# Optimization experiments

Measured on AMD Instinct MI355X. Metric: run time of the kernel, lower is better.

## Reference

```python
import jax, jax.numpy as jnp
import numpy as np

B, N, DIM = 2, 2048, 1024
H, DH = 16, 64
INNER = H * DH
SCALE = DH ** -0.5


def rotate_half(x):
    x1, x2 = jnp.split(x, 2, axis=-1)
    return jnp.concatenate((-x2, x1), axis=-1)


def apply_rotary(pos, t):
    # pos: [n, dh] broadcast against t: [b, h, n, dh]
    return t * jnp.cos(pos) + rotate_half(t) * jnp.sin(pos)


def setup_inputs() -> dict:
    key = jax.random.key(0)
    ks = jax.random.split(key, 5)
    x = jax.random.normal(ks[0], (B, N, DIM), dtype=jnp.float32)
    rotary_emb = jax.random.normal(ks[1], (N, DH), dtype=jnp.float32)
    w_qkv = jax.random.normal(ks[2], (3 * INNER, DIM), dtype=jnp.float32) * (DIM ** -0.5)
    w_out = jax.random.normal(ks[3], (DIM, INNER), dtype=jnp.float32) * (INNER ** -0.5)
    b_out = jax.random.normal(ks[4], (DIM,), dtype=jnp.float32) * 0.01
    return {"x": x, "rotary_emb": rotary_emb, "w_qkv": w_qkv, "w_out": w_out, "b_out": b_out}


def reference(x, rotary_emb, w_qkv, w_out, b_out):
    b, n, _ = x.shape
    qkv = jnp.einsum('bnd,ed->bne', x, w_qkv)  # [b, n, 3*inner]
    q, k, v = jnp.split(qkv, 3, axis=-1)
    # [b, n, inner] -> [b, h, n, dh]
    reshape = lambda t: t.reshape(b, n, H, DH).transpose(0, 2, 1, 3)
    q, k, v = reshape(q), reshape(k), reshape(v)
    q = apply_rotary(rotary_emb, q)
    k = apply_rotary(rotary_emb, k)
    dots = jnp.einsum('bhid,bhjd->bhij', q, k) * SCALE
    attn = jax.nn.softmax(dots, axis=-1)
    out = jnp.einsum('bhij,bhjd->bhid', attn, v)
    out = out.transpose(0, 2, 1, 3).reshape(b, n, INNER)
    return jnp.einsum('bne,de->bnd', out, w_out) + b_out
```

## Files before the change

### kernel.cpp

```cpp
#include <hip/hip_runtime.h>
#include <math.h>

typedef unsigned short ushort_t;
typedef __attribute__((ext_vector_type(8))) short short8v;
typedef __attribute__((ext_vector_type(4))) float float4v;

#define BB 2
#define NN 2048
#define HH 16
#define DHH 64
#define DIMM 1024
#define QKV3 3072
#define INNERR 1024
#define QSCALE 0.1803368801111244f

__device__ __forceinline__ ushort_t f2bf(float f) {
    unsigned u = __float_as_uint(f);
    u += 0x7fffu + ((u >> 16) & 1u);
    return (ushort_t)(u >> 16);
}
__device__ __forceinline__ float bf2f(unsigned h) {
    return __uint_as_float(h << 16);
}
__device__ __forceinline__ unsigned pk_bf16(float a, float b) {
#if __has_builtin(__builtin_amdgcn_cvt_pk_bf16_f32)
    typedef __attribute__((ext_vector_type(2))) __bf16 bf16x2;
    bf16x2 r = __builtin_amdgcn_cvt_pk_bf16_f32(a, b);
    return __builtin_bit_cast(unsigned, r);
#else
    return (unsigned)f2bf(a) | ((unsigned)f2bf(b) << 16);
#endif
}
__device__ __forceinline__ float fast_exp2(float x) {
#if __has_builtin(__builtin_amdgcn_exp2f)
    return __builtin_amdgcn_exp2f(x);
#else
    return exp2f(x);
#endif
}
__device__ __forceinline__ float fast_rcp(float x) {
#if __has_builtin(__builtin_amdgcn_rcpf)
    return __builtin_amdgcn_rcpf(x);
#else
    return 1.0f / x;
#endif
}
__device__ __forceinline__ void gl2lds16(const void* g, void* l) {
    __builtin_amdgcn_global_load_lds(
        (const __attribute__((address_space(1))) unsigned int*)g,
        (__attribute__((address_space(3))) unsigned int*)l, 16, 0, 0);
}

__global__ __launch_bounds__(256) void conv_fused(const float* __restrict__ wqkv,
                                                  const float* __restrict__ wout,
                                                  ushort_t* __restrict__ wqkvo,
                                                  ushort_t* __restrict__ wouto) {
    int blk = blockIdx.x;
    const float* in; ushort_t* out; int i;
    if (blk < 3072) { in = wqkv; out = wqkvo; i = blk * 256 + threadIdx.x; }
    else            { in = wout; out = wouto; i = (blk - 3072) * 256 + threadIdx.x; }
    float4 v = ((const float4*)in)[i];
    ushort4 o;
    o.x = f2bf(v.x); o.y = f2bf(v.y); o.z = f2bf(v.z); o.w = f2bf(v.w);
    ((ushort4*)out)[i] = o;
}

__global__ __launch_bounds__(256, 3) void gemm1_rot(const float* __restrict__ Ax,
                                                    const ushort_t* __restrict__ Bm,
                                                    const float* __restrict__ rot,
                                                    ushort_t* __restrict__ Vt,
                                                    ushort_t* __restrict__ Cout, int K) {
    __shared__ float    Asf[2][128 * 32];
    __shared__ ushort_t Bs[2][128 * 32];
    const int t = threadIdx.x;
    const int lane = t & 63;
    const int w = t >> 6;
    const int wr = w >> 1;
    const int wc = w & 1;
    const int quad = lane >> 4;
    const int l15 = lane & 15;
    const int m0 = blockIdx.y * 128;
    const int n0 = blockIdx.x * 128;

    float4v acc[4][4];
#pragma unroll
    for (int i = 0; i < 4; ++i)
#pragma unroll
        for (int j = 0; j < 4; ++j) acc[i][j] = (float4v)0.0f;

    int row_[6], lcv[6], dst[6];
#pragma unroll
    for (int u = 0; u < 6; ++u) {
        int c = u * 256 + t;
        if (u < 4) {
            int row = c >> 3;
            row_[u] = row;
            lcv[u] = (c & 7) ^ (row & 7);
            dst[u] = c * 4;
        } else {
            int cb = c - 1024;
            int row = cb >> 2;
            row_[u] = row;
            lcv[u] = (cb & 3) ^ ((row >> 1) & 3);
            dst[u] = cb * 8;
        }
    }
#pragma unroll
    for (int u = 0; u < 6; ++u) {
        if (u < 4) gl2lds16(&Ax[(size_t)(m0 + row_[u]) * K + lcv[u] * 4], &Asf[0][dst[u]]);
        else       gl2lds16(&Bm[(size_t)(n0 + row_[u]) * K + lcv[u] * 8], &Bs[0][dst[u]]);
    }
    const int NIT = K >> 5;
    for (int it = 0; it < NIT; ++it) {
        const int cur = it & 1;
        if (it + 1 < NIT) {
            const int nxt = cur ^ 1;
            const int kc = (it + 1) << 5;
#pragma unroll
            for (int u = 0; u < 6; ++u) {
                if (u < 4) gl2lds16(&Ax[(size_t)(m0 + row_[u]) * K + kc + lcv[u] * 4], &Asf[nxt][dst[u]]);
                else       gl2lds16(&Bm[(size_t)(n0 + row_[u]) * K + kc + lcv[u] * 8], &Bs[nxt][dst[u]]);
            }
            asm volatile("s_waitcnt vmcnt(6)\n\ts_barrier" ::: "memory");
        } else {
            asm volatile("s_waitcnt vmcnt(0)\n\ts_barrier" ::: "memory");
        }
        short8v a[4], b[4];
#pragma unroll
        for (int i = 0; i < 4; ++i) {
            int row = wr * 64 + i * 16 + l15;
            int r7 = row & 7;
            float4v raw0 = *(const float4v*)&Asf[cur][row * 32 + ((2 * quad) ^ r7) * 4];
            float4v raw1 = *(const float4v*)&Asf[cur][row * 32 + ((2 * quad + 1) ^ r7) * 4];
            uint4 u_;
            u_.x = pk_bf16(raw0[0], raw0[1]); u_.y = pk_bf16(raw0[2], raw0[3]);
            u_.z = pk_bf16(raw1[0], raw1[1]); u_.w = pk_bf16(raw1[2], raw1[3]);
            a[i] = __builtin_bit_cast(short8v, u_);
        }
#pragma unroll
        for (int j = 0; j < 4; ++j) {
            int row = wc * 64 + j * 16 + l15;
            int pc = quad ^ ((row >> 1) & 3);
            b[j] = *(const short8v*)&Bs[cur][row * 32 + pc * 8];
        }
#pragma unroll
        for (int i = 0; i < 4; ++i)
#pragma unroll
            for (int j = 0; j < 4; ++j)
                acc[i][j] = __builtin_amdgcn_mfma_f32_16x16x32_bf16(a[i], b[j], acc[i][j], 0, 0, 0);
        asm volatile("s_barrier" ::: "memory");
    }
    const int region = n0 >> 10;
    if (region == 2) {
#pragma unroll
        for (int i = 0; i < 4; ++i) {
            int grow = m0 + wr * 64 + i * 16 + quad * 4;
            int bb = grow >> 11, nn_ = grow & (NN - 1);
            int tk = nn_ & 63;
            int tp = (tk & 32) | ((tk & 12) << 1) | ((tk & 16) >> 2);
            int nstore = (nn_ & ~63) | tp;
#pragma unroll
            for (int j = 0; j < 4; ++j) {
                int vcol = n0 + wc * 64 + j * 16 + l15 - 2048;
                int hh = vcol >> 6, dh = vcol & 63;
                uint2 st;
                st.x = pk_bf16(acc[i][j][0], acc[i][j][1]);
                st.y = pk_bf16(acc[i][j][2], acc[i][j][3]);
                *(uint2*)&Vt[((size_t)(bb * HH + hh) * DHH + dh) * NN + nstore] = st;
            }
        }
        return;
    }
    {
        float scale = (region == 0) ? QSCALE : 1.0f;
#pragma unroll
        for (int i = 0; i < 4; ++i) {
#pragma unroll
            for (int r = 0; r < 4; ++r) {
                int n = (m0 + wr * 64 + i * 16 + quad * 4 + r) & (NN - 1);
#pragma unroll
                for (int jl = 0; jl < 2; ++jl) {
                    int dh = jl * 16 + l15;
                    float plo = rot[n * DHH + dh];
                    float phi = rot[n * DHH + dh + 32];
                    float lo = acc[i][jl][r], hi = acc[i][jl + 2][r];
                    acc[i][jl][r]     = (lo * __cosf(plo) - hi * __sinf(plo)) * scale;
                    acc[i][jl + 2][r] = (hi * __cosf(phi) + lo * __sinf(phi)) * scale;
                }
            }
        }
    }
#pragma unroll
    for (int i = 0; i < 4; ++i) {
        int grow = m0 + wr * 64 + i * 16 + quad * 4;
#pragma unroll
        for (int j = 0; j < 4; ++j) {
            int gcol = n0 + wc * 64 + j * 16 + l15;
#pragma unroll
            for (int r = 0; r < 4; ++r)
                Cout[(size_t)(grow + r) * QKV3 + gcol] = f2bf(acc[i][j][r]);
        }
    }
}

template <int NOUT, bool BIAS>
__global__ __launch_bounds__(256, 4) void gemm_64(const ushort_t* __restrict__ A,
                                                  const ushort_t* __restrict__ Bm,
                                                  const float* __restrict__ bias,
                                                  float* __restrict__ Cout, int K) {
    __shared__ ushort_t As[2][64 * 64];
    __shared__ ushort_t Bs[2][64 * 64];
    const int t = threadIdx.x;
    const int lane = t & 63;
    const int w = t >> 6;
    const int wr = w >> 1;
    const int wc = w & 1;
    const int quad = lane >> 4;
    const int l15 = lane & 15;
    const int m0 = blockIdx.y * 64;
    const int n0 = blockIdx.x * 64;

    float4v acc[2][2];
#pragma unroll
    for (int i = 0; i < 2; ++i)
#pragma unroll
        for (int j = 0; j < 2; ++j) acc[i][j] = (float4v)0.0f;

    int row_[4], lcv[4], dst[4];
#pragma unroll
    for (int u = 0; u < 4; ++u) {
        int c = u * 256 + t;
        int cb = (u < 2) ? c : (c - 512);
        int row = cb >> 3;
        row_[u] = row;
        lcv[u] = (cb & 7) ^ (row & 7);
        dst[u] = cb * 8;
    }
#pragma unroll
    for (int u = 0; u < 4; ++u) {
        if (u < 2) gl2lds16(&A[(size_t)(m0 + row_[u]) * K + lcv[u] * 8], &As[0][dst[u]]);
        else       gl2lds16(&Bm[(size_t)(n0 + row_[u]) * K + lcv[u] * 8], &Bs[0][dst[u]]);
    }
    const int NIT = K >> 6;
    for (int it = 0; it < NIT; ++it) {
        const int cur = it & 1;
        if (it + 1 < NIT) {
            const int nxt = cur ^ 1;
            const int kc = (it + 1) << 6;
#pragma unroll
            for (int u = 0; u < 4; ++u) {
                if (u < 2) gl2lds16(&A[(size_t)(m0 + row_[u]) * K + kc + lcv[u] * 8], &As[nxt][dst[u]]);
                else       gl2lds16(&Bm[(size_t)(n0 + row_[u]) * K + kc + lcv[u] * 8], &Bs[nxt][dst[u]]);
            }
            asm volatile("s_waitcnt vmcnt(4)\n\ts_barrier" ::: "memory");
        } else {
            asm volatile("s_waitcnt vmcnt(0)\n\ts_barrier" ::: "memory");
        }
        short8v a[2][2], b[2][2];
#pragma unroll
        for (int i = 0; i < 2; ++i) {
            int row = wr * 32 + i * 16 + l15;
            int r7 = row & 7;
            a[0][i] = *(const short8v*)&As[cur][row * 64 + ((quad) ^ r7) * 8];
            a[1][i] = *(const short8v*)&As[cur][row * 64 + ((4 + quad) ^ r7) * 8];
        }
#pragma unroll
        for (int j = 0; j < 2; ++j) {
            int row = wc * 32 + j * 16 + l15;
            int r7 = row & 7;
            b[0][j] = *(const short8v*)&Bs[cur][row * 64 + ((quad) ^ r7) * 8];
            b[1][j] = *(const short8v*)&Bs[cur][row * 64 + ((4 + quad) ^ r7) * 8];
        }
#pragma unroll
        for (int kh = 0; kh < 2; ++kh)
#pragma unroll
            for (int i = 0; i < 2; ++i)
#pragma unroll
                for (int j = 0; j < 2; ++j)
                    acc[i][j] = __builtin_amdgcn_mfma_f32_16x16x32_bf16(a[kh][i], b[kh][j], acc[i][j], 0, 0, 0);
        asm volatile("s_barrier" ::: "memory");
    }
#pragma unroll
    for (int i = 0; i < 2; ++i) {
        int grow = m0 + wr * 32 + i * 16 + quad * 4;
#pragma unroll
        for (int j = 0; j < 2; ++j) {
            int gcol = n0 + wc * 32 + j * 16 + l15;
            float bv = BIAS ? bias[gcol] : 0.0f;
#pragma unroll
            for (int r = 0; r < 4; ++r)
                Cout[(size_t)(grow + r) * NOUT + gcol] = acc[i][j][r] + bv;
        }
    }
}

__global__ __launch_bounds__(256, 2) void flash_mfma(const ushort_t* __restrict__ qkv,
                                                     const ushort_t* __restrict__ Vt,
                                                     ushort_t* __restrict__ attn) {
    __shared__ ushort_t smem[16384];
    const int t = threadIdx.x;
    const int lane = t & 63;
    const int w = t >> 6;
    const int quad = lane >> 4;
    const int l15 = lane & 15;
    const int blk = blockIdx.x;
    const int slot = blk >> 3;
    const int qt = slot & 15;
    const int bh = (blk & 7) * 4 + (slot >> 4);
    const int b = bh >> 4, h = bh & 15;
    const int n0 = qt * 128;

    short8v bq[2][2];
#pragma unroll
    for (int g = 0; g < 2; ++g) {
        size_t qb = (size_t)(b * NN + n0 + w * 32 + g * 16 + l15) * QKV3 + h * DHH + quad * 8;
        bq[g][0] = *(const short8v*)&qkv[qb];
        bq[g][1] = *(const short8v*)&qkv[qb + 32];
    }
    float4v o_acc[2][4];
    float4v l_acc[2];
#pragma unroll
    for (int g = 0; g < 2; ++g) {
        l_acc[g] = (float4v)0.0f;
#pragma unroll
        for (int nb = 0; nb < 4; ++nb) o_acc[g][nb] = (float4v)0.0f;
    }
    const short one_bf = (short)0x3F80;
    short8v ones8 = {one_bf, one_bf, one_bf, one_bf, one_bf, one_bf, one_bf, one_bf};
    const float4v ZR = (float4v)0.0f;

    const int s0 = t, s1 = 256 + t;
    const int r0 = s0 >> 3, lc0 = (s0 & 7) ^ (r0 & 7);
    const int r1 = s1 >> 3, lc1 = (s1 & 7) ^ (r1 & 7);
    const int koff0 = r0 * QKV3 + lc0 * 8, koff1 = r1 * QKV3 + lc1 * 8;
    const int voff0 = r0 * NN + lc0 * 8,   voff1 = r1 * NN + lc1 * 8;
    const ushort_t* kp = qkv + (size_t)b * NN * QKV3 + INNERR + h * DHH;
    const ushort_t* vp = Vt + (size_t)(b * HH + h) * DHH * NN;

    {
        gl2lds16(kp + koff0, smem + 0 * 4096 + s0 * 8);
        gl2lds16(kp + koff1, smem + 0 * 4096 + s1 * 8);
        gl2lds16(vp + voff0, smem + 2 * 4096 + s0 * 8);
        gl2lds16(vp + voff1, smem + 2 * 4096 + s1 * 8);
    }
    for (int jt = 0; jt < 32; ++jt) {
        const int cur = jt & 1;
        if (jt < 31) {
            kp += 64 * QKV3;
            vp += 64;
            const int nxt = cur ^ 1;
            gl2lds16(kp + koff0, smem + nxt * 4096 + s0 * 8);
            gl2lds16(kp + koff1, smem + nxt * 4096 + s1 * 8);
            gl2lds16(vp + voff0, smem + (2 + nxt) * 4096 + s0 * 8);
            gl2lds16(vp + voff1, smem + (2 + nxt) * 4096 + s1 * 8);
            asm volatile("s_waitcnt vmcnt(4)\n\ts_barrier" ::: "memory");
        } else {
            asm volatile("s_waitcnt vmcnt(0)\n\ts_barrier" ::: "memory");
        }
        const ushort_t* Ksc = smem + cur * 4096;
        const ushort_t* Vtc = smem + (2 + cur) * 4096;
        short8v ak[2][4], bv[2][4];
#pragma unroll
        for (int nb = 0; nb < 4; ++nb) {
            int row = nb * 16 + l15;
            int base = row * 64;
            int r7 = row & 7;
            ak[0][nb] = *(const short8v*)&Ksc[base + ((quad) ^ r7) * 8];
            ak[1][nb] = *(const short8v*)&Ksc[base + ((4 + quad) ^ r7) * 8];
            bv[0][nb] = *(const short8v*)&Vtc[base + ((quad) ^ r7) * 8];
            bv[1][nb] = *(const short8v*)&Vtc[base + ((4 + quad) ^ r7) * 8];
        }
        __builtin_amdgcn_s_setprio(1);
        float4v s0v[4], s1v[4];
#pragma unroll
        for (int nb = 0; nb < 4; ++nb)
            s0v[nb] = __builtin_amdgcn_mfma_f32_16x16x32_bf16(ak[0][nb], bq[0][0], ZR, 0, 0, 0);
#pragma unroll
        for (int nb = 0; nb < 4; ++nb)
            s0v[nb] = __builtin_amdgcn_mfma_f32_16x16x32_bf16(ak[1][nb], bq[0][1], s0v[nb], 0, 0, 0);
#pragma unroll
        for (int nb = 0; nb < 4; ++nb)
            s1v[nb] = __builtin_amdgcn_mfma_f32_16x16x32_bf16(ak[0][nb], bq[1][0], ZR, 0, 0, 0);
#pragma unroll
        for (int nb = 0; nb < 4; ++nb)
            s1v[nb] = __builtin_amdgcn_mfma_f32_16x16x32_bf16(ak[1][nb], bq[1][1], s1v[nb], 0, 0, 0);
#pragma unroll
        for (int g = 0; g < 2; ++g) {
            float4v* sv = (g == 0) ? s0v : s1v;
            float p[4][4];
#pragma unroll
            for (int nb = 0; nb < 4; ++nb)
#pragma unroll
                for (int r = 0; r < 4; ++r) p[nb][r] = fast_exp2(sv[nb][r]);
            uint4 u0, u1;
            u0.x = pk_bf16(p[0][0], p[0][1]); u0.y = pk_bf16(p[0][2], p[0][3]);
            u0.z = pk_bf16(p[1][0], p[1][1]); u0.w = pk_bf16(p[1][2], p[1][3]);
            u1.x = pk_bf16(p[2][0], p[2][1]); u1.y = pk_bf16(p[2][2], p[2][3]);
            u1.z = pk_bf16(p[3][0], p[3][1]); u1.w = pk_bf16(p[3][2], p[3][3]);
            short8v ap0 = __builtin_bit_cast(short8v, u0);
            short8v ap1 = __builtin_bit_cast(short8v, u1);
            l_acc[g] = __builtin_amdgcn_mfma_f32_16x16x32_bf16(ap0, ones8, l_acc[g], 0, 0, 0);
            l_acc[g] = __builtin_amdgcn_mfma_f32_16x16x32_bf16(ap1, ones8, l_acc[g], 0, 0, 0);
#pragma unroll
            for (int nb = 0; nb < 4; ++nb) {
                o_acc[g][nb] = __builtin_amdgcn_mfma_f32_16x16x32_bf16(ap0, bv[0][nb], o_acc[g][nb], 0, 0, 0);
                o_acc[g][nb] = __builtin_amdgcn_mfma_f32_16x16x32_bf16(ap1, bv[1][nb], o_acc[g][nb], 0, 0, 0);
            }
        }
        __builtin_amdgcn_s_setprio(0);
        asm volatile("s_barrier" ::: "memory");
    }
    float inv[2][4];
#pragma unroll
    for (int g = 0; g < 2; ++g)
#pragma unroll
        for (int r = 0; r < 4; ++r) inv[g][r] = fast_rcp(l_acc[g][r]);
    ushort_t* osc = smem + w * (32 * 68);
#pragma unroll
    for (int g = 0; g < 2; ++g)
#pragma unroll
        for (int nb = 0; nb < 4; ++nb)
#pragma unroll
            for (int r = 0; r < 4; ++r)
                osc[(g * 16 + quad * 4 + r) * 68 + nb * 16 + l15] = f2bf(o_acc[g][nb][r] * inv[g][r]);
    __builtin_amdgcn_s_waitcnt(0);
    {
        int rr = lane >> 1, c0 = (lane & 1) * 32;
        size_t arow = ((size_t)(b * NN + n0 + w * 32 + rr)) * INNERR + h * DHH + c0;
#pragma unroll
        for (int u = 0; u < 4; ++u) {
            uint4 v = *(const uint4*)&osc[rr * 68 + c0 + u * 8];
            *(uint4*)&attn[arow + u * 8] = v;
        }
    }
}

extern "C" void kernel_launch(void* const* d_in, const int* in_sizes, int n_in,
                              void* d_out, int out_size, void* d_ws, size_t ws_size,
                              hipStream_t stream) {
    const float* x = (const float*)d_in[0];
    const float* rot = (const float*)d_in[1];
    const float* w_qkv = (const float*)d_in[2];
    const float* w_out = (const float*)d_in[3];
    const float* b_out = (const float*)d_in[4];
    float* y = (float*)d_out;

    char* ws = (char*)d_ws;
    ushort_t* qkv_bf  = (ushort_t*)(ws);
    ushort_t* vt_bf   = (ushort_t*)(ws + 25165824);
    ushort_t* wout_bf = (ushort_t*)(ws + 33554432);
    ushort_t* wqkv_bf = (ushort_t*)(ws + 35651584);
    ushort_t* attn_bf = (ushort_t*)(ws + 41943040);

    conv_fused<<<4096, 256, 0, stream>>>(w_qkv, w_out, wqkv_bf, wout_bf);
    gemm1_rot<<<dim3(24, 32), 256, 0, stream>>>(
        x, wqkv_bf, rot, vt_bf, qkv_bf, DIMM);
    flash_mfma<<<512, 256, 0, stream>>>(qkv_bf, vt_bf, attn_bf);
    gemm_64<INNERR, true><<<dim3(16, 64), 256, 0, stream>>>(
        attn_bf, wout_bf, b_out, y, INNERR);
}
```

Measured before the change: 183.8 us.

## Pre-convert x to bf16 in conversion kernel and swizzle GEMM1 block order

Moves the fp32-to-bf16 conversion of x out of the QKV GEMM's inner loop into the existing weight-conversion kernel, so the GEMM loads bf16 A tiles straight into LDS. This halves the A-tile global and LDS traffic and drops the per-iteration packing ALU work, at the cost of an extra pass that writes and rereads x in bf16. It also remaps the 1D grid with an XCD-aware swizzle so neighbouring tiles share L2, and reuses the attention-output buffer as the x_bf scratch.

```diff
diff --git a/kernel.cpp b/kernel.cpp
--- a/kernel.cpp
+++ b/kernel.cpp
@@ -51,26 +51,30 @@
         (__attribute__((address_space(3))) unsigned int*)l, 16, 0, 0);
 }
 
-__global__ __launch_bounds__(256) void conv_fused(const float* __restrict__ wqkv,
+__global__ __launch_bounds__(256) void conv_fused(const float* __restrict__ x,
+                                                  const float* __restrict__ wqkv,
                                                   const float* __restrict__ wout,
+                                                  ushort_t* __restrict__ xo,
                                                   ushort_t* __restrict__ wqkvo,
                                                   ushort_t* __restrict__ wouto) {
     int blk = blockIdx.x;
     const float* in; ushort_t* out; int i;
-    if (blk < 3072) { in = wqkv; out = wqkvo; i = blk * 256 + threadIdx.x; }
-    else            { in = wout; out = wouto; i = (blk - 3072) * 256 + threadIdx.x; }
+    if (blk < 4096)      { in = x;    out = xo;    i = blk * 256 + threadIdx.x; }
+    else if (blk < 7168) { in = wqkv; out = wqkvo; i = (blk - 4096) * 256 + threadIdx.x; }
+    else                 { in = wout; out = wouto; i = (blk - 7168) * 256 + threadIdx.x; }
     float4 v = ((const float4*)in)[i];
     ushort4 o;
     o.x = f2bf(v.x); o.y = f2bf(v.y); o.z = f2bf(v.z); o.w = f2bf(v.w);
     ((ushort4*)out)[i] = o;
 }
 
-__global__ __launch_bounds__(256, 3) void gemm1_rot(const float* __restrict__ Ax,
+__global__ __launch_bounds__(256, 3) void gemm1_rot(const ushort_t* __restrict__ A,
                                                     const ushort_t* __restrict__ Bm,
                                                     const float* __restrict__ rot,
                                                     ushort_t* __restrict__ Vt,
                                                     ushort_t* __restrict__ Cout, int K) {
-    __shared__ float    Asf[2][128 * 32];
+    constexpr int NCH = 4;
+    __shared__ ushort_t As[2][128 * 32];
     __shared__ ushort_t Bs[2][128 * 32];
     const int t = threadIdx.x;
     const int lane = t & 63;
@@ -79,8 +83,10 @@
     const int wc = w & 1;
     const int quad = lane >> 4;
     const int l15 = lane & 15;
-    const int m0 = blockIdx.y * 128;
-    const int n0 = blockIdx.x * 128;
+    const int lid = blockIdx.x;
+    const int swz = (lid & 7) * 96 + (lid >> 3);
+    const int m0 = (swz / 24) * 128;
+    const int n0 = (swz % 24) * 128;
 
     float4v acc[4][4];
 #pragma unroll
@@ -88,27 +94,24 @@
 #pragma unroll
         for (int j = 0; j < 4; ++j) acc[i][j] = (float4v)0.0f;
 
-    int row_[6], lcv[6], dst[6];
-#pragma unroll
-    for (int u = 0; u < 6; ++u) {
+    int srow[NCH], slc[NCH], sdst[NCH];
+    bool sisA[NCH];
+#pragma unroll
+    for (int u = 0; u < NCH; ++u) {
         int c = u * 256 + t;
-        if (u < 4) {
-            int row = c >> 3;
-            row_[u] = row;
-            lcv[u] = (c & 7) ^ (row & 7);
-            dst[u] = c * 4;
+        if (c < 512) {
+            int row = c >> 2;
+            sisA[u] = true; srow[u] = row; slc[u] = (c & 3) ^ ((row >> 1) & 3); sdst[u] = c * 8;
         } else {
-            int cb = c - 1024;
+            int cb = c - 512;
             int row = cb >> 2;
-            row_[u] = row;
-            lcv[u] = (cb & 3) ^ ((row >> 1) & 3);
-            dst[u] = cb * 8;
-        }
-    }
-#pragma unroll
-    for (int u = 0; u < 6; ++u) {
-        if (u < 4) gl2lds16(&Ax[(size_t)(m0 + row_[u]) * K + lcv[u] * 4], &Asf[0][dst[u]]);
-        else       gl2lds16(&Bm[(size_t)(n0 + row_[u]) * K + lcv[u] * 8], &Bs[0][dst[u]]);
+            sisA[u] = false; srow[u] = row; slc[u] = (cb & 3) ^ ((row >> 1) & 3); sdst[u] = cb * 8;
+        }
+    }
+#pragma unroll
+    for (int u = 0; u < NCH; ++u) {
+        if (sisA[u]) gl2lds16(&A[(size_t)(m0 + srow[u]) * K + slc[u] * 8], &As[0][sdst[u]]);
+        else         gl2lds16(&Bm[(size_t)(n0 + srow[u]) * K + slc[u] * 8], &Bs[0][sdst[u]]);
     }
     const int NIT = K >> 5;
     for (int it = 0; it < NIT; ++it) {
@@ -117,11 +120,11 @@
             const int nxt = cur ^ 1;
             const int kc = (it + 1) << 5;
 #pragma unroll
-            for (int u = 0; u < 6; ++u) {
-                if (u < 4) gl2lds16(&Ax[(size_t)(m0 + row_[u]) * K + kc + lcv[u] * 4], &Asf[nxt][dst[u]]);
-                else       gl2lds16(&Bm[(size_t)(n0 + row_[u]) * K + kc + lcv[u] * 8], &Bs[nxt][dst[u]]);
+            for (int u = 0; u < NCH; ++u) {
+                if (sisA[u]) gl2lds16(&A[(size_t)(m0 + srow[u]) * K + kc + slc[u] * 8], &As[nxt][sdst[u]]);
+                else         gl2lds16(&Bm[(size_t)(n0 + srow[u]) * K + kc + slc[u] * 8], &Bs[nxt][sdst[u]]);
             }
-            asm volatile("s_waitcnt vmcnt(6)\n\ts_barrier" ::: "memory");
+            asm volatile("s_waitcnt vmcnt(4)\n\ts_barrier" ::: "memory");
         } else {
             asm volatile("s_waitcnt vmcnt(0)\n\ts_barrier" ::: "memory");
         }
@@ -129,13 +132,8 @@
 #pragma unroll
         for (int i = 0; i < 4; ++i) {
             int row = wr * 64 + i * 16 + l15;
-            int r7 = row & 7;
-            float4v raw0 = *(const float4v*)&Asf[cur][row * 32 + ((2 * quad) ^ r7) * 4];
-            float4v raw1 = *(const float4v*)&Asf[cur][row * 32 + ((2 * quad + 1) ^ r7) * 4];
-            uint4 u_;
-            u_.x = pk_bf16(raw0[0], raw0[1]); u_.y = pk_bf16(raw0[2], raw0[3]);
-            u_.z = pk_bf16(raw1[0], raw1[1]); u_.w = pk_bf16(raw1[2], raw1[3]);
-            a[i] = __builtin_bit_cast(short8v, u_);
+            int pc = quad ^ ((row >> 1) & 3);
+            a[i] = *(const short8v*)&As[cur][row * 32 + pc * 8];
         }
 #pragma unroll
         for (int j = 0; j < 4; ++j) {
@@ -450,11 +448,12 @@
     ushort_t* vt_bf   = (ushort_t*)(ws + 25165824);
     ushort_t* wout_bf = (ushort_t*)(ws + 33554432);
     ushort_t* wqkv_bf = (ushort_t*)(ws + 35651584);
-    ushort_t* attn_bf = (ushort_t*)(ws + 41943040);
-
-    conv_fused<<<4096, 256, 0, stream>>>(w_qkv, w_out, wqkv_bf, wout_bf);
-    gemm1_rot<<<dim3(24, 32), 256, 0, stream>>>(
-        x, wqkv_bf, rot, vt_bf, qkv_bf, DIMM);
+    ushort_t* x_bf    = (ushort_t*)(ws + 41943040);
+    ushort_t* attn_bf = x_bf;
+
+    conv_fused<<<8192, 256, 0, stream>>>(x, w_qkv, w_out, x_bf, wqkv_bf, wout_bf);
+    gemm1_rot<<<768, 256, 0, stream>>>(
+        x_bf, wqkv_bf, rot, vt_bf, qkv_bf, DIMM);
     flash_mfma<<<512, 256, 0, stream>>>(qkv_bf, vt_bf, attn_bf);
     gemm_64<INNERR, true><<<dim3(16, 64), 256, 0, stream>>>(
         attn_bf, wout_bf, b_out, y, INNERR);
```

New measurement: 175.1 us (median of 2 runs). 4.7% less time.
